# Optimization experiments

Measured on AMD Instinct MI355X. Metric: run time of the kernel, lower is better.

## Reference

```python
import jax, jax.numpy as jnp
import numpy as np

N, K, CL, CP = 8192, 32, 384, 128   # residues, neighbours, local dim, pair dim
H, S, P = 4, 32, 8                   # heads, head size, query points


def setup_inputs() -> dict:
    key = jax.random.key(0)
    ks = jax.random.split(key, 12)

    def lin(k, fi, fo):
        return jax.random.normal(k, (fi, fo), jnp.float32) / jnp.sqrt(jnp.float32(fi))

    return {
        "local": jax.random.normal(ks[0], (N, CL), jnp.float32),
        "pair": jax.random.normal(ks[1], (N, K, CP), jnp.float32),
        "frames": jax.random.normal(ks[2], (N, 4, 4), jnp.float32),
        "neighbours": jax.random.randint(ks[3], (N, K), 0, N),
        "mask": jnp.ones((N, K), dtype=bool),
        "Wq": lin(ks[4], CL, H * S), "bq": jnp.zeros((H * S,), jnp.float32),
        "Wk": lin(ks[5], CL, S), "bk": jnp.zeros((S,), jnp.float32),
        "Wv": lin(ks[6], CL, S), "bv": jnp.zeros((S,), jnp.float32),
        "Wqp": lin(ks[7], CL, H * P * 3), "bqp": jnp.zeros((H * P * 3,), jnp.float32),
        "Wkp": lin(ks[8], CL, P * 3), "bkp": jnp.zeros((P * 3,), jnp.float32),
        "Wvp": lin(ks[9], CL, P * 3), "bvp": jnp.zeros((P * 3,), jnp.float32),
        "Wb": lin(ks[10], CP, H),
        "gamma": jnp.full((H,), np.log(np.exp(1.0) - 1.0), jnp.float32),
        "Wout": lin(ks[11], H * S + H * CP + H * P * 3, CL),
    }


def _ln(x):
    # hk.LayerNorm([-1], create_scale=False, create_offset=False), eps=1e-5
    m = x.mean(-1, keepdims=True)
    v = ((x - m) ** 2).mean(-1, keepdims=True)
    return (x - m) * jax.lax.rsqrt(v + 1e-5)


def reference(local, pair, frames, neighbours, mask,
              Wq, bq, Wk, bk, Wv, bv, Wqp, bqp, Wkp, bkp, Wvp, bvp,
              Wb, gamma, Wout):
    frames = frames.astype(jnp.float32)
    rot = frames[:, :3, :3]       # (N,3,3)
    trans = frames[:, :3, 3]      # (N,3)
    n = local.shape[0]

    q = _ln((local @ Wq + bq).reshape(n, H, S))   # (N,H,S)
    k = _ln(local @ Wk + bk)                      # (N,S)  single (shared) head
    v = local @ Wv + bv                           # (N,S)

    def pts(W, b, h):
        p = (local @ W + b).reshape(n, h, P, 3)
        # frames[:,None,None].apply_to_point: rot @ p + trans
        return jnp.einsum('nab,nhpb->nhpa', rot, p) + trans[:, None, None, :]

    qp = pts(Wqp, bqp, H)            # (N,H,P,3)
    kp = pts(Wkp, bkp, 1)[:, 0]      # (N,P,3)
    vp = pts(Wvp, bvp, 1)[:, 0]      # (N,P,3)

    w_C = jnp.sqrt(2.0 / (9.0 * P))
    w_L = jnp.sqrt(1.0 / 3.0)
    scale = jax.nn.softplus(gamma)[None, None, :] * w_C / 2   # (1,1,H)

    logits = jnp.einsum('nhc,nkc->nkh', q / jnp.sqrt(jnp.float32(S)), k[neighbours])
    diff = qp[:, None] - kp[neighbours][:, :, None]           # (N,K,H,P,3)
    dist = (diff ** 2).sum((-1, -2))                          # (N,K,H)
    logits = w_L * (logits - scale * dist + pair @ Wb)
    logits = jnp.where(mask[..., None], logits, -1e9)
    attn = jax.nn.softmax(logits, axis=1)
    attn = jnp.where(mask[..., None], attn, 0)

    local_up = jnp.einsum('nkh,nkc->nhc', attn, v[neighbours]).reshape(n, -1)
    pair_up = jnp.einsum('nkh,nkc->nhc', attn, pair).reshape(n, -1)
    pt = jnp.einsum('nkh,nkpa->nhpa', attn, vp[neighbours])   # (N,H,P,3)
    # apply_inverse_to_point: rot^T @ (x - trans)
    pt = jnp.einsum('nba,nhpb->nhpa', rot, pt - trans[:, None, None, :])

    result = jnp.concatenate([local_up, pair_up, pt.reshape(n, -1)], axis=-1)
    return result @ Wout
```

## Files before the change

kernel.cpp:

```cpp
#include <hip/hip_runtime.h>
#include <hip/hip_bf16.h>

#define NN 8192
#define KK 32
#define CL 384
#define CP 128
#define HH 4
#define SS 32
#define PP 8
#define PW 336
#define RW 736

#define FMA4(ac, s, b) { (ac).x += (s)*(b).x; (ac).y += (s)*(b).y; (ac).z += (s)*(b).z; (ac).w += (s)*(b).w; }

typedef __attribute__((ext_vector_type(8))) short bf16x8_t;
typedef __attribute__((ext_vector_type(4))) float f32x4_t;

__device__ __forceinline__ unsigned short f2bf_rne(float x) {
  unsigned int u = __float_as_uint(x);
  u += 0x7fffu + ((u >> 16) & 1u);
  return (unsigned short)(u >> 16);
}
__device__ __forceinline__ float bf2f(unsigned short h) {
  return __uint_as_float(((unsigned int)h) << 16);
}

__global__ void pack_bt(const float* __restrict__ Wq, const float* __restrict__ Wk,
                        const float* __restrict__ Wv, const float* __restrict__ Wqp,
                        const float* __restrict__ Wkp, const float* __restrict__ Wvp,
                        const float* __restrict__ Wout,
                        const float* __restrict__ bq, const float* __restrict__ bk,
                        const float* __restrict__ bv, const float* __restrict__ bqp,
                        const float* __restrict__ bkp, const float* __restrict__ bvp,
                        unsigned short* __restrict__ Bt1h, unsigned short* __restrict__ Bt1l,
                        unsigned short* __restrict__ Bt2h, unsigned short* __restrict__ Bt2l,
                        float* __restrict__ b_all) {
  const int bid = blockIdx.x, tid = threadIdx.x;
  if (bid < PW) {
    const int n = bid;
    for (int k = tid; k < CL; k += 128) {
      float x;
      if (n < 128)      x = Wq[k * 128 + n];
      else if (n < 160) x = Wk[k * 32 + (n - 128)];
      else if (n < 192) x = Wv[k * 32 + (n - 160)];
      else if (n < 288) x = Wqp[k * 96 + (n - 192)];
      else if (n < 312) x = Wkp[k * 24 + (n - 288)];
      else              x = Wvp[k * 24 + (n - 312)];
      unsigned short h = f2bf_rne(x);
      Bt1h[n * CL + k] = h;
      Bt1l[n * CL + k] = f2bf_rne(x - bf2f(h));
    }
    if (bid == 0) {
      for (int j = tid; j < PW; j += 128) {
        float b;
        if (j < 128)      b = bq[j];
        else if (j < 160) b = bk[j - 128];
        else if (j < 192) b = bv[j - 160];
        else if (j < 288) b = bqp[j - 192];
        else if (j < 312) b = bkp[j - 288];
        else              b = bvp[j - 312];
        b_all[j] = b;
      }
    }
  } else {
    const int n = bid - PW;
    for (int k = tid; k < RW; k += 128) {
      float x = Wout[k * CL + n];
      unsigned short h = f2bf_rne(x);
      Bt2h[n * RW + k] = h;
      Bt2l[n * RW + k] = f2bf_rne(x - bf2f(h));
    }
  }
}

template<bool BIAS>
__global__ __launch_bounds__(256) void gemm_bf16s(
    const float* __restrict__ A,
    const unsigned short* __restrict__ BtHi, const unsigned short* __restrict__ BtLo,
    const float* __restrict__ bias, float* __restrict__ C,
    int M, int Kd, int Nc) {
  __shared__ unsigned short Ah[2048], Al[2048], Bh[2048], Bl[2048];
  const int tid = threadIdx.x;
  const int lane = tid & 63;
  const int w = tid >> 6;
  const int wm = w >> 1, wn = w & 1;
  const int m0 = blockIdx.y * 64, n0 = blockIdx.x * 64;

  const int arow = tid >> 3;
  const int akq = (tid & 7) * 4;
  const int bn = tid >> 2;
  const int bk8 = (tid & 3) * 8;
  const bool bok = (n0 + bn) < Nc;
  const int NT = Kd / 32;

  float4 va[2];
  uint4 vbh, vbl;

#pragma unroll
  for (int u = 0; u < 2; ++u)
    va[u] = *(const float4*)(A + (size_t)(m0 + arow + u * 32) * Kd + akq);
  if (bok) {
    vbh = *(const uint4*)(BtHi + (size_t)(n0 + bn) * Kd + bk8);
    vbl = *(const uint4*)(BtLo + (size_t)(n0 + bn) * Kd + bk8);
  } else {
    vbh = make_uint4(0, 0, 0, 0);
    vbl = make_uint4(0, 0, 0, 0);
  }

  f32x4_t acc[2][2];
#pragma unroll
  for (int i = 0; i < 2; ++i)
#pragma unroll
    for (int j = 0; j < 2; ++j) acc[i][j] = (f32x4_t)0.0f;

  for (int t = 0; t < NT; ++t) {
#pragma unroll
    for (int u = 0; u < 2; ++u) {
      int m = arow + u * 32;
      int idx = (m >> 4) * 512 + ((akq >> 3) * 16 + (m & 15)) * 8 + (akq & 7);
      float xs[4] = {va[u].x, va[u].y, va[u].z, va[u].w};
      unsigned short hh[4], ll[4];
#pragma unroll
      for (int j = 0; j < 4; ++j) {
        hh[j] = f2bf_rne(xs[j]);
        ll[j] = f2bf_rne(xs[j] - bf2f(hh[j]));
      }
      *(uint2*)&Ah[idx] = make_uint2((unsigned)hh[0] | ((unsigned)hh[1] << 16),
                                     (unsigned)hh[2] | ((unsigned)hh[3] << 16));
      *(uint2*)&Al[idx] = make_uint2((unsigned)ll[0] | ((unsigned)ll[1] << 16),
                                     (unsigned)ll[2] | ((unsigned)ll[3] << 16));
    }
    {
      int idx = (bn >> 4) * 512 + ((bk8 >> 3) * 16 + (bn & 15)) * 8;
      *(uint4*)&Bh[idx] = vbh;
      *(uint4*)&Bl[idx] = vbl;
    }
    __syncthreads();

    if (t + 1 < NT) {
      const int k0 = (t + 1) * 32;
#pragma unroll
      for (int u = 0; u < 2; ++u)
        va[u] = *(const float4*)(A + (size_t)(m0 + arow + u * 32) * Kd + k0 + akq);
      if (bok) {
        vbh = *(const uint4*)(BtHi + (size_t)(n0 + bn) * Kd + k0 + bk8);
        vbl = *(const uint4*)(BtLo + (size_t)(n0 + bn) * Kd + k0 + bk8);
      } else {
        vbh = make_uint4(0, 0, 0, 0);
        vbl = make_uint4(0, 0, 0, 0);
      }
    }

    {
      bf16x8_t ah[2], al[2], bh[2], bl[2];
#pragma unroll
      for (int nr = 0; nr < 2; ++nr) {
        int fb = wn * 2 + nr;
        bh[nr] = *(const bf16x8_t*)&Bh[fb * 512 + lane * 8];
        bl[nr] = *(const bf16x8_t*)&Bl[fb * 512 + lane * 8];
      }
#pragma unroll
      for (int mr = 0; mr < 2; ++mr) {
        int fa = wm * 2 + mr;
        ah[mr] = *(const bf16x8_t*)&Ah[fa * 512 + lane * 8];
        al[mr] = *(const bf16x8_t*)&Al[fa * 512 + lane * 8];
      }
#pragma unroll
      for (int mr = 0; mr < 2; ++mr)
#pragma unroll
        for (int nr = 0; nr < 2; ++nr) {
          acc[mr][nr] = __builtin_amdgcn_mfma_f32_16x16x32_bf16(ah[mr], bh[nr], acc[mr][nr], 0, 0, 0);
          acc[mr][nr] = __builtin_amdgcn_mfma_f32_16x16x32_bf16(ah[mr], bl[nr], acc[mr][nr], 0, 0, 0);
          acc[mr][nr] = __builtin_amdgcn_mfma_f32_16x16x32_bf16(al[mr], bh[nr], acc[mr][nr], 0, 0, 0);
        }
    }
    __syncthreads();
  }

#pragma unroll
  for (int mr = 0; mr < 2; ++mr) {
#pragma unroll
    for (int nr = 0; nr < 2; ++nr) {
      int col = n0 + wn * 32 + nr * 16 + (lane & 15);
      if (col < Nc) {
        int rowb = m0 + wm * 32 + mr * 16 + (lane >> 4) * 4;
        float badd = BIAS ? bias[col] : 0.f;
#pragma unroll
        for (int r = 0; r < 4; ++r)
          C[(size_t)(rowb + r) * Nc + col] = acc[mr][nr][r] + badd;
      }
    }
  }
}

__global__ __launch_bounds__(256) void transform_kernel(
    const float* __restrict__ proj, const float* __restrict__ frames,
    float* __restrict__ feats) {
  int lane = threadIdx.x & 63;
  int node = blockIdx.x * 4 + (threadIdx.x >> 6);
  const float* pr = proj + (size_t)node * PW;
  float* fr = feats + (size_t)node * PW;
  const float* F = frames + (size_t)node * 16;
  int j = lane & 31;
#pragma unroll
  for (int pass = 0; pass < 2; ++pass) {
    int h = pass * 2 + (lane >> 5);
    float x = pr[h * 32 + j];
    float s = x;
#pragma unroll
    for (int m = 16; m >= 1; m >>= 1) s += __shfl_xor(s, m, 32);
    float mean = s * (1.f / 32.f);
    float d = x - mean;
    float vs = d * d;
#pragma unroll
    for (int m = 16; m >= 1; m >>= 1) vs += __shfl_xor(vs, m, 32);
    fr[h * 32 + j] = d / sqrtf(vs * (1.f / 32.f) + 1e-5f);
  }
  if (lane < 32) {
    float x = pr[128 + j];
    float s = x;
#pragma unroll
    for (int m = 16; m >= 1; m >>= 1) s += __shfl_xor(s, m, 32);
    float mean = s * (1.f / 32.f);
    float d = x - mean;
    float vs = d * d;
#pragma unroll
    for (int m = 16; m >= 1; m >>= 1) vs += __shfl_xor(vs, m, 32);
    fr[128 + j] = d / sqrtf(vs * (1.f / 32.f) + 1e-5f);
  } else {
    fr[160 + j] = pr[160 + j];
  }
  if (lane < 48) {
    int c = 192 + lane * 3;
    float x = pr[c], y = pr[c + 1], z = pr[c + 2];
#pragma unroll
    for (int a = 0; a < 3; ++a)
      fr[c + a] = F[a*4+0]*x + F[a*4+1]*y + F[a*4+2]*z + F[a*4+3];
  }
}

__global__ __launch_bounds__(256) void attn_kernel(
    const float* __restrict__ feats, const float* __restrict__ pair,
    const int* __restrict__ neighbours, const float* __restrict__ frames,
    const float* __restrict__ Wb, const float* __restrict__ gamma,
    float* __restrict__ result) {
  const int n = blockIdx.x;
  const int tid = threadIdx.x;
  __shared__ float q_s[4 * 36];
  __shared__ float qp_s[96];
  __shared__ float kv_s[32 * 68];
  __shared__ float kpvp_s[32 * 52];
  __shared__ float bias_s[128];
  __shared__ float attn_s[128];
  __shared__ float red_s[16], red2_s[16];
  __shared__ float pt_s[96];

  const float* fr = feats + (size_t)n * PW;
  const float* pbase = pair + (size_t)n * (KK * CP);
  float* out = result + (size_t)n * RW;

  if (tid < 128) q_s[(tid >> 5) * 36 + (tid & 31)] = fr[tid];
  else if (tid < 224) qp_s[tid - 128] = fr[192 + (tid - 128)];
  {
    const int k = tid >> 3, r = tid & 7;
    const int nbk = neighbours[n * KK + k];
    const float* src = feats + (size_t)nbk * PW;
    float4 v0 = *(const float4*)(src + 128 + r * 8);
    float4 v1 = *(const float4*)(src + 128 + r * 8 + 4);
    *(float4*)&kv_s[k * 68 + r * 8] = v0;
    *(float4*)&kv_s[k * 68 + r * 8 + 4] = v1;
#pragma unroll
    for (int i = 0; i < 6; ++i) kpvp_s[k * 52 + r * 6 + i] = src[288 + r * 6 + i];

    const float* pg = pbase + k * CP + r * 16;
    float4 p0 = *(const float4*)(pg);
    float4 p1 = *(const float4*)(pg + 4);
    float4 p2 = *(const float4*)(pg + 8);
    float4 p3 = *(const float4*)(pg + 12);
    float pv[16] = {p0.x,p0.y,p0.z,p0.w, p1.x,p1.y,p1.z,p1.w,
                    p2.x,p2.y,p2.z,p2.w, p3.x,p3.y,p3.z,p3.w};
    const float4* Wb4 = (const float4*)Wb;
    float4 b4 = make_float4(0.f, 0.f, 0.f, 0.f);
#pragma unroll
    for (int i = 0; i < 16; ++i) {
      float4 wv = Wb4[r * 16 + i];
      FMA4(b4, pv[i], wv);
    }
#pragma unroll
    for (int m = 1; m <= 4; m <<= 1) {
      b4.x += __shfl_xor(b4.x, m);
      b4.y += __shfl_xor(b4.y, m);
      b4.z += __shfl_xor(b4.z, m);
      b4.w += __shfl_xor(b4.w, m);
    }
    if (r == 0) *(float4*)&bias_s[k * 4] = b4;
  }
  __syncthreads();

  {
    const int lk = tid >> 3, lh = (tid >> 1) & 3, le = tid & 1;
    float qk = 0.f;
#pragma unroll
    for (int j = 0; j < 4; ++j) {
      float4 qv = *(const float4*)&q_s[lh * 36 + le * 16 + j * 4];
      float4 kv = *(const float4*)&kv_s[lk * 68 + le * 16 + j * 4];
      qk += qv.x*kv.x + qv.y*kv.y + qv.z*kv.z + qv.w*kv.w;
    }
    float dist = 0.f;
#pragma unroll
    for (int j = 0; j < 3; ++j) {
      float4 qpv = *(const float4*)&qp_s[lh * 24 + le * 12 + j * 4];
      float4 kpv = *(const float4*)&kpvp_s[lk * 52 + le * 12 + j * 4];
      float d0 = qpv.x - kpv.x, d1 = qpv.y - kpv.y;
      float d2 = qpv.z - kpv.z, d3 = qpv.w - kpv.w;
      dist += d0*d0 + d1*d1 + d2*d2 + d3*d3;
    }
    float scale = log1pf(__expf(gamma[lh])) * (1.f / 12.f);
    float part = qk * 0.17677669529663687f - scale * dist;
    part += __shfl_xor(part, 1);
    float logit = 0.57735026918962576f * (part + bias_s[lk * 4 + lh]);
    float mw = logit;
#pragma unroll
    for (int m = 8; m <= 32; m <<= 1) mw = fmaxf(mw, __shfl_xor(mw, m));
    const int w = tid >> 6;
    if ((tid & 63) == lh * 2) red_s[w * 4 + lh] = mw;
    __syncthreads();
    float mx = fmaxf(fmaxf(red_s[lh], red_s[4 + lh]),
                     fmaxf(red_s[8 + lh], red_s[12 + lh]));
    float p = __expf(logit - mx);
    float sw = p;
#pragma unroll
    for (int m = 8; m <= 32; m <<= 1) sw += __shfl_xor(sw, m);
    if ((tid & 63) == lh * 2) red2_s[w * 4 + lh] = sw;
    __syncthreads();
    float denom = red2_s[lh] + red2_s[4 + lh] + red2_s[8 + lh] + red2_s[12 + lh];
    if (le == 0) attn_s[lk * 4 + lh] = p / denom;
  }
  __syncthreads();

  if (tid < 128) {
    const int h = tid >> 5, c4 = (tid & 31) * 4;
    const float* pgk = pbase + c4;
    float4 acc = make_float4(0.f, 0.f, 0.f, 0.f);
#pragma unroll
    for (int k = 0; k < 32; ++k) {
      float av = attn_s[k * 4 + h];
      float4 pv = *(const float4*)(pgk + k * CP);
      FMA4(acc, av, pv);
    }
    *(float4*)(out + 128 + h * 128 + c4) = acc;
  } else if (tid < 160) {
    const int idx = tid - 128;
    const int h = idx >> 3, c4 = (idx & 7) * 4;
    float4 acc = make_float4(0.f, 0.f, 0.f, 0.f);
#pragma unroll
    for (int k = 0; k < 32; ++k) {
      float av = attn_s[k * 4 + h];
      float4 vv = *(const float4*)&kv_s[k * 68 + 32 + c4];
      FMA4(acc, av, vv);
    }
    *(float4*)(out + h * 32 + c4) = acc;
  } else if (tid < 184) {
    const int idx = tid - 160;
    const int h = idx / 6, q6 = (idx % 6) * 4;
    float4 acc = make_float4(0.f, 0.f, 0.f, 0.f);
#pragma unroll
    for (int k = 0; k < 32; ++k) {
      float av = attn_s[k * 4 + h];
      float4 vv = *(const float4*)&kpvp_s[k * 52 + 24 + q6];
      FMA4(acc, av, vv);
    }
    *(float4*)&pt_s[h * 24 + q6] = acc;
  }
  __syncthreads();

  if (tid < 96) {
    const int h = tid / 24, rr = tid % 24, pp = rr / 3, aa = rr % 3;
    const float* F = frames + (size_t)n * 16;
    float s = 0.f;
#pragma unroll
    for (int b = 0; b < 3; ++b)
      s += F[b * 4 + aa] * (pt_s[h * 24 + pp * 3 + b] - F[b * 4 + 3]);
    out[640 + tid] = s;
  }
}

extern "C" void kernel_launch(void* const* d_in, const int* in_sizes, int n_in,
                              void* d_out, int out_size, void* d_ws, size_t ws_size,
                              hipStream_t stream) {
  (void)in_sizes; (void)n_in; (void)out_size; (void)ws_size;
  const float* local      = (const float*)d_in[0];
  const float* pair       = (const float*)d_in[1];
  const float* frames     = (const float*)d_in[2];
  const int*   neighbours = (const int*)d_in[3];
  const float* Wq   = (const float*)d_in[5];
  const float* bq   = (const float*)d_in[6];
  const float* Wk   = (const float*)d_in[7];
  const float* bk   = (const float*)d_in[8];
  const float* Wv   = (const float*)d_in[9];
  const float* bv   = (const float*)d_in[10];
  const float* Wqp  = (const float*)d_in[11];
  const float* bqp  = (const float*)d_in[12];
  const float* Wkp  = (const float*)d_in[13];
  const float* bkp  = (const float*)d_in[14];
  const float* Wvp  = (const float*)d_in[15];
  const float* bvp  = (const float*)d_in[16];
  const float* Wb   = (const float*)d_in[17];
  const float* gamma= (const float*)d_in[18];
  const float* Wout = (const float*)d_in[19];

  float* ws     = (float*)d_ws;
  float* b_all  = ws;
  float* proj   = ws + 352;
  float* feats  = proj + (size_t)NN * PW;
  float* result = feats + (size_t)NN * PW;
  unsigned short* Bt1h = (unsigned short*)(result + (size_t)NN * RW);
  unsigned short* Bt1l = Bt1h + PW * CL;
  unsigned short* Bt2h = Bt1l + PW * CL;
  unsigned short* Bt2l = Bt2h + CL * RW;
  float* out    = (float*)d_out;

  hipLaunchKernelGGL(pack_bt, dim3(PW + CL), dim3(128), 0, stream,
                     Wq, Wk, Wv, Wqp, Wkp, Wvp, Wout,
                     bq, bk, bv, bqp, bkp, bvp,
                     Bt1h, Bt1l, Bt2h, Bt2l, b_all);
  hipLaunchKernelGGL((gemm_bf16s<true>), dim3((PW + 63) / 64, NN / 64), dim3(256), 0, stream,
                     local, Bt1h, Bt1l, b_all, proj, NN, CL, PW);
  hipLaunchKernelGGL(transform_kernel, dim3(NN / 4), dim3(256), 0, stream,
                     proj, frames, feats);
  hipLaunchKernelGGL(attn_kernel, dim3(NN), dim3(256), 0, stream,
                     feats, pair, neighbours, frames, Wb, gamma, result);
  hipLaunchKernelGGL((gemm_bf16s<false>), dim3(CL / 64, NN / 64), dim3(256), 0, stream,
                     result, Bt2h, Bt2l, nullptr, out, NN, RW, CL);
}
```

Before: 343.8 us.

## Pre-pack GEMM operands into MFMA fragment layout and drop LDS staging

Weights are now packed into 16x32 MFMA fragment order, and a new conv_pack kernel converts the fp32 activations into split hi/lo bf16 fragments before each GEMM. The GEMM then loads fragments straight from global memory with register double-buffering, so it needs no LDS, no __syncthreads and no in-loop fp32-to-bf16 conversion. Blocks are remapped with a grouped swizzle to improve cache reuse. The cost is two extra kernel launches and an extra global round-trip for the packed activations, and B fragments are no longer shared across waves through LDS.

New measurement: 359.3 us. 4.5% more time.

```diff
diff --git a/kernel.cpp b/kernel.cpp
--- a/kernel.cpp
+++ b/kernel.cpp
@@ -10,34 +10,39 @@
 #define PP 8
 #define PW 336
 #define RW 736
+#define FK1 12
+#define FK2 23
+#define NF1 21
+#define NF2 24
 
 #define FMA4(ac, s, b) { (ac).x += (s)*(b).x; (ac).y += (s)*(b).y; (ac).z += (s)*(b).z; (ac).w += (s)*(b).w; }
 
 typedef __attribute__((ext_vector_type(8))) short bf16x8_t;
 typedef __attribute__((ext_vector_type(4))) float f32x4_t;
-
-__device__ __forceinline__ unsigned short f2bf_rne(float x) {
+typedef unsigned short ush;
+
+__device__ __forceinline__ ush f2bf_rne(float x) {
   unsigned int u = __float_as_uint(x);
   u += 0x7fffu + ((u >> 16) & 1u);
-  return (unsigned short)(u >> 16);
-}
-__device__ __forceinline__ float bf2f(unsigned short h) {
+  return (ush)(u >> 16);
+}
+__device__ __forceinline__ float bf2f(ush h) {
   return __uint_as_float(((unsigned int)h) << 16);
 }
 
-__global__ void pack_bt(const float* __restrict__ Wq, const float* __restrict__ Wk,
-                        const float* __restrict__ Wv, const float* __restrict__ Wqp,
-                        const float* __restrict__ Wkp, const float* __restrict__ Wvp,
-                        const float* __restrict__ Wout,
-                        const float* __restrict__ bq, const float* __restrict__ bk,
-                        const float* __restrict__ bv, const float* __restrict__ bqp,
-                        const float* __restrict__ bkp, const float* __restrict__ bvp,
-                        unsigned short* __restrict__ Bt1h, unsigned short* __restrict__ Bt1l,
-                        unsigned short* __restrict__ Bt2h, unsigned short* __restrict__ Bt2l,
-                        float* __restrict__ b_all) {
+__global__ void pack_b_frag(const float* __restrict__ Wq, const float* __restrict__ Wk,
+                            const float* __restrict__ Wv, const float* __restrict__ Wqp,
+                            const float* __restrict__ Wkp, const float* __restrict__ Wvp,
+                            const float* __restrict__ Wout,
+                            const float* __restrict__ bq, const float* __restrict__ bk,
+                            const float* __restrict__ bv, const float* __restrict__ bqp,
+                            const float* __restrict__ bkp, const float* __restrict__ bvp,
+                            ush* __restrict__ B1h, ush* __restrict__ B1l,
+                            ush* __restrict__ B2h, ush* __restrict__ B2l,
+                            float* __restrict__ b_all) {
   const int bid = blockIdx.x, tid = threadIdx.x;
   if (bid < PW) {
-    const int n = bid;
+    const int n = bid, fn = n >> 4, nr = n & 15;
     for (int k = tid; k < CL; k += 128) {
       float x;
       if (n < 128)      x = Wq[k * 128 + n];
@@ -46,9 +51,11 @@
       else if (n < 288) x = Wqp[k * 96 + (n - 192)];
       else if (n < 312) x = Wkp[k * 24 + (n - 288)];
       else              x = Wvp[k * 24 + (n - 312)];
-      unsigned short h = f2bf_rne(x);
-      Bt1h[n * CL + k] = h;
-      Bt1l[n * CL + k] = f2bf_rne(x - bf2f(h));
+      ush h = f2bf_rne(x);
+      int lane = nr | (((k >> 3) & 3) << 4);
+      size_t idx = ((size_t)fn * FK1 + (k >> 5)) * 512 + lane * 8 + (k & 7);
+      B1h[idx] = h;
+      B1l[idx] = f2bf_rne(x - bf2f(h));
     }
     if (bid == 0) {
       for (int j = tid; j < PW; j += 128) {
@@ -63,133 +70,119 @@
       }
     }
   } else {
-    const int n = bid - PW;
+    const int n = bid - PW, fn = n >> 4, nr = n & 15;
     for (int k = tid; k < RW; k += 128) {
       float x = Wout[k * CL + n];
-      unsigned short h = f2bf_rne(x);
-      Bt2h[n * RW + k] = h;
-      Bt2l[n * RW + k] = f2bf_rne(x - bf2f(h));
-    }
-  }
-}
-
-template<bool BIAS>
-__global__ __launch_bounds__(256) void gemm_bf16s(
-    const float* __restrict__ A,
-    const unsigned short* __restrict__ BtHi, const unsigned short* __restrict__ BtLo,
-    const float* __restrict__ bias, float* __restrict__ C,
-    int M, int Kd, int Nc) {
-  __shared__ unsigned short Ah[2048], Al[2048], Bh[2048], Bl[2048];
-  const int tid = threadIdx.x;
-  const int lane = tid & 63;
-  const int w = tid >> 6;
-  const int wm = w >> 1, wn = w & 1;
-  const int m0 = blockIdx.y * 64, n0 = blockIdx.x * 64;
-
-  const int arow = tid >> 3;
-  const int akq = (tid & 7) * 4;
-  const int bn = tid >> 2;
-  const int bk8 = (tid & 3) * 8;
-  const bool bok = (n0 + bn) < Nc;
-  const int NT = Kd / 32;
-
-  float4 va[2];
-  uint4 vbh, vbl;
-
-#pragma unroll
-  for (int u = 0; u < 2; ++u)
-    va[u] = *(const float4*)(A + (size_t)(m0 + arow + u * 32) * Kd + akq);
-  if (bok) {
-    vbh = *(const uint4*)(BtHi + (size_t)(n0 + bn) * Kd + bk8);
-    vbl = *(const uint4*)(BtLo + (size_t)(n0 + bn) * Kd + bk8);
-  } else {
-    vbh = make_uint4(0, 0, 0, 0);
-    vbl = make_uint4(0, 0, 0, 0);
-  }
-
-  f32x4_t acc[2][2];
-#pragma unroll
-  for (int i = 0; i < 2; ++i)
-#pragma unroll
-    for (int j = 0; j < 2; ++j) acc[i][j] = (f32x4_t)0.0f;
-
-  for (int t = 0; t < NT; ++t) {
-#pragma unroll
-    for (int u = 0; u < 2; ++u) {
-      int m = arow + u * 32;
-      int idx = (m >> 4) * 512 + ((akq >> 3) * 16 + (m & 15)) * 8 + (akq & 7);
-      float xs[4] = {va[u].x, va[u].y, va[u].z, va[u].w};
-      unsigned short hh[4], ll[4];
-#pragma unroll
-      for (int j = 0; j < 4; ++j) {
-        hh[j] = f2bf_rne(xs[j]);
-        ll[j] = f2bf_rne(xs[j] - bf2f(hh[j]));
+      ush h = f2bf_rne(x);
+      int lane = nr | (((k >> 3) & 3) << 4);
+      size_t idx = ((size_t)fn * FK2 + (k >> 5)) * 512 + lane * 8 + (k & 7);
+      B2h[idx] = h;
+      B2l[idx] = f2bf_rne(x - bf2f(h));
+    }
+  }
+}
+
+template<int KD>
+__global__ __launch_bounds__(256) void conv_pack(const float* __restrict__ A,
+                                                 ush* __restrict__ Ph,
+                                                 ush* __restrict__ Pl) {
+  constexpr int FK = KD / 32;
+  const int lane = threadIdx.x & 63;
+  const int fm = blockIdx.x * 4 + (threadIdx.x >> 6);
+  const int fk = blockIdx.y;
+  const int r = lane >> 2, kq = lane & 3;
+  const float* src = A + (size_t)(fm * 16 + r) * KD + fk * 32 + kq * 8;
+  float4 v0 = *(const float4*)src;
+  float4 v1 = *(const float4*)(src + 4);
+  float xs[8] = {v0.x, v0.y, v0.z, v0.w, v1.x, v1.y, v1.z, v1.w};
+  ush hh[8], ll[8];
+#pragma unroll
+  for (int j = 0; j < 8; ++j) {
+    hh[j] = f2bf_rne(xs[j]);
+    ll[j] = f2bf_rne(xs[j] - bf2f(hh[j]));
+  }
+  const int lw = r | (kq << 4);
+  size_t base = ((size_t)fm * FK + fk) * 512 + lw * 8;
+  uint4 vh, vl;
+  vh.x = (unsigned)hh[0] | ((unsigned)hh[1] << 16);
+  vh.y = (unsigned)hh[2] | ((unsigned)hh[3] << 16);
+  vh.z = (unsigned)hh[4] | ((unsigned)hh[5] << 16);
+  vh.w = (unsigned)hh[6] | ((unsigned)hh[7] << 16);
+  vl.x = (unsigned)ll[0] | ((unsigned)ll[1] << 16);
+  vl.y = (unsigned)ll[2] | ((unsigned)ll[3] << 16);
+  vl.z = (unsigned)ll[4] | ((unsigned)ll[5] << 16);
+  vl.w = (unsigned)ll[6] | ((unsigned)ll[7] << 16);
+  *(uint4*)&Ph[base] = vh;
+  *(uint4*)&Pl[base] = vl;
+}
+
+template<int FK, bool BIAS>
+__global__ __launch_bounds__(128) void gemm_pk(
+    const ush* __restrict__ Aph, const ush* __restrict__ Apl,
+    const ush* __restrict__ Bph, const ush* __restrict__ Bpl,
+    const float* __restrict__ bias, float* __restrict__ C, int Nc) {
+  const int lane = threadIdx.x & 63;
+  const int wv = threadIdx.x >> 6;
+  const int nbx = gridDim.x;
+  const int nb = nbx * gridDim.y;
+  const int lin = blockIdx.y * nbx + blockIdx.x;
+  const int q = nb >> 3;
+  const int wg = (lin & 7) * q + (lin >> 3);
+  const int fn = wg % nbx;
+  const int mb = wg / nbx;
+  const int fm0 = mb * 8 + wv * 4;
+
+  const ush* bhp = Bph + ((size_t)fn * FK) * 512 + lane * 8;
+  const ush* blp = Bpl + ((size_t)fn * FK) * 512 + lane * 8;
+  const ush* ahp = Aph + ((size_t)fm0 * FK) * 512 + lane * 8;
+  const ush* alp = Apl + ((size_t)fm0 * FK) * 512 + lane * 8;
+  const size_t AS = (size_t)FK * 512;
+
+  f32x4_t acc[4];
+#pragma unroll
+  for (int i = 0; i < 4; ++i) acc[i] = (f32x4_t)0.0f;
+
+  bf16x8_t nbh = *(const bf16x8_t*)bhp;
+  bf16x8_t nbl = *(const bf16x8_t*)blp;
+  bf16x8_t nah[4], nal[4];
+#pragma unroll
+  for (int mr = 0; mr < 4; ++mr) {
+    nah[mr] = *(const bf16x8_t*)(ahp + mr * AS);
+    nal[mr] = *(const bf16x8_t*)(alp + mr * AS);
+  }
+
+  for (int fk = 0; fk < FK; ++fk) {
+    bf16x8_t cbh = nbh, cbl = nbl;
+    bf16x8_t cah[4], cal[4];
+#pragma unroll
+    for (int mr = 0; mr < 4; ++mr) { cah[mr] = nah[mr]; cal[mr] = nal[mr]; }
+    if (fk + 1 < FK) {
+      const size_t o = (size_t)(fk + 1) * 512;
+      nbh = *(const bf16x8_t*)(bhp + o);
+      nbl = *(const bf16x8_t*)(blp + o);
+#pragma unroll
+      for (int mr = 0; mr < 4; ++mr) {
+        nah[mr] = *(const bf16x8_t*)(ahp + mr * AS + o);
+        nal[mr] = *(const bf16x8_t*)(alp + mr * AS + o);
       }
-      *(uint2*)&Ah[idx] = make_uint2((unsigned)hh[0] | ((unsigned)hh[1] << 16),
-                                     (unsigned)hh[2] | ((unsigned)hh[3] << 16));
-      *(uint2*)&Al[idx] = make_uint2((unsigned)ll[0] | ((unsigned)ll[1] << 16),
-                                     (unsigned)ll[2] | ((unsigned)ll[3] << 16));
-    }
-    {
-      int idx = (bn >> 4) * 512 + ((bk8 >> 3) * 16 + (bn & 15)) * 8;
-      *(uint4*)&Bh[idx] = vbh;
-      *(uint4*)&Bl[idx] = vbl;
-    }
-    __syncthreads();
-
-    if (t + 1 < NT) {
-      const int k0 = (t + 1) * 32;
-#pragma unroll
-      for (int u = 0; u < 2; ++u)
-        va[u] = *(const float4*)(A + (size_t)(m0 + arow + u * 32) * Kd + k0 + akq);
-      if (bok) {
-        vbh = *(const uint4*)(BtHi + (size_t)(n0 + bn) * Kd + k0 + bk8);
-        vbl = *(const uint4*)(BtLo + (size_t)(n0 + bn) * Kd + k0 + bk8);
-      } else {
-        vbh = make_uint4(0, 0, 0, 0);
-        vbl = make_uint4(0, 0, 0, 0);
-      }
-    }
-
-    {
-      bf16x8_t ah[2], al[2], bh[2], bl[2];
-#pragma unroll
-      for (int nr = 0; nr < 2; ++nr) {
-        int fb = wn * 2 + nr;
-        bh[nr] = *(const bf16x8_t*)&Bh[fb * 512 + lane * 8];
-        bl[nr] = *(const bf16x8_t*)&Bl[fb * 512 + lane * 8];
-      }
-#pragma unroll
-      for (int mr = 0; mr < 2; ++mr) {
-        int fa = wm * 2 + mr;
-        ah[mr] = *(const bf16x8_t*)&Ah[fa * 512 + lane * 8];
-        al[mr] = *(const bf16x8_t*)&Al[fa * 512 + lane * 8];
-      }
-#pragma unroll
-      for (int mr = 0; mr < 2; ++mr)
-#pragma unroll
-        for (int nr = 0; nr < 2; ++nr) {
-          acc[mr][nr] = __builtin_amdgcn_mfma_f32_16x16x32_bf16(ah[mr], bh[nr], acc[mr][nr], 0, 0, 0);
-          acc[mr][nr] = __builtin_amdgcn_mfma_f32_16x16x32_bf16(ah[mr], bl[nr], acc[mr][nr], 0, 0, 0);
-          acc[mr][nr] = __builtin_amdgcn_mfma_f32_16x16x32_bf16(al[mr], bh[nr], acc[mr][nr], 0, 0, 0);
-        }
-    }
-    __syncthreads();
-  }
-
-#pragma unroll
-  for (int mr = 0; mr < 2; ++mr) {
-#pragma unroll
-    for (int nr = 0; nr < 2; ++nr) {
-      int col = n0 + wn * 32 + nr * 16 + (lane & 15);
-      if (col < Nc) {
-        int rowb = m0 + wm * 32 + mr * 16 + (lane >> 4) * 4;
-        float badd = BIAS ? bias[col] : 0.f;
-#pragma unroll
-        for (int r = 0; r < 4; ++r)
-          C[(size_t)(rowb + r) * Nc + col] = acc[mr][nr][r] + badd;
-      }
-    }
+    }
+#pragma unroll
+    for (int mr = 0; mr < 4; ++mr) {
+      acc[mr] = __builtin_amdgcn_mfma_f32_16x16x32_bf16(cah[mr], cbh, acc[mr], 0, 0, 0);
+      acc[mr] = __builtin_amdgcn_mfma_f32_16x16x32_bf16(cah[mr], cbl, acc[mr], 0, 0, 0);
+      acc[mr] = __builtin_amdgcn_mfma_f32_16x16x32_bf16(cal[mr], cbh, acc[mr], 0, 0, 0);
+    }
+  }
+
+  const int col = fn * 16 + (lane & 15);
+  const float badd = BIAS ? bias[col] : 0.f;
+  const int rsub = (lane >> 4) * 4;
+#pragma unroll
+  for (int mr = 0; mr < 4; ++mr) {
+    const int row = (fm0 + mr) * 16 + rsub;
+#pragma unroll
+    for (int rr = 0; rr < 4; ++rr)
+      C[(size_t)(row + rr) * Nc + col] = acc[mr][rr] + badd;
   }
 }
 
@@ -414,22 +407,28 @@
   float* proj   = ws + 352;
   float* feats  = proj + (size_t)NN * PW;
   float* result = feats + (size_t)NN * PW;
-  unsigned short* Bt1h = (unsigned short*)(result + (size_t)NN * RW);
-  unsigned short* Bt1l = Bt1h + PW * CL;
-  unsigned short* Bt2h = Bt1l + PW * CL;
-  unsigned short* Bt2l = Bt2h + CL * RW;
-  float* out    = (float*)d_out;
-
-  hipLaunchKernelGGL(pack_bt, dim3(PW + CL), dim3(128), 0, stream,
+  ush* Apkh = (ush*)(result + (size_t)NN * RW);
+  ush* Apkl = Apkh + (size_t)NN * RW;
+  ush* B1h  = Apkl + (size_t)NN * RW;
+  ush* B1l  = B1h + NF1 * FK1 * 512;
+  ush* B2h  = B1l + NF1 * FK1 * 512;
+  ush* B2l  = B2h + NF2 * FK2 * 512;
+  float* out = (float*)d_out;
+
+  hipLaunchKernelGGL(pack_b_frag, dim3(PW + CL), dim3(128), 0, stream,
                      Wq, Wk, Wv, Wqp, Wkp, Wvp, Wout,
                      bq, bk, bv, bqp, bkp, bvp,
-                     Bt1h, Bt1l, Bt2h, Bt2l, b_all);
-  hipLaunchKernelGGL((gemm_bf16s<true>), dim3((PW + 63) / 64, NN / 64), dim3(256), 0, stream,
-                     local, Bt1h, Bt1l, b_all, proj, NN, CL, PW);
+                     B1h, B1l, B2h, B2l, b_all);
+  hipLaunchKernelGGL((conv_pack<CL>), dim3(NN / 64, FK1), dim3(256), 0, stream,
+                     local, Apkh, Apkl);
+  hipLaunchKernelGGL((gemm_pk<FK1, true>), dim3(NF1, NN / 128), dim3(128), 0, stream,
+                     Apkh, Apkl, B1h, B1l, b_all, proj, PW);
   hipLaunchKernelGGL(transform_kernel, dim3(NN / 4), dim3(256), 0, stream,
                      proj, frames, feats);
   hipLaunchKernelGGL(attn_kernel, dim3(NN), dim3(256), 0, stream,
                      feats, pair, neighbours, frames, Wb, gamma, result);
-  hipLaunchKernelGGL((gemm_bf16s<false>), dim3(CL / 64, NN / 64), dim3(256), 0, stream,
-                     result, Bt2h, Bt2l, nullptr, out, NN, RW, CL);
-}
+  hipLaunchKernelGGL((conv_pack<RW>), dim3(NN / 64, FK2), dim3(256), 0, stream,
+                     result, Apkh, Apkl);
+  hipLaunchKernelGGL((gemm_pk<FK2, false>), dim3(NF2, NN / 128), dim3(128), 0, stream,
+                     Apkh, Apkl, B2h, B2l, nullptr, out, CL);
+}
```
